# Optimization experiments

Measured on AMD Instinct MI355X. Metric: run time of the kernel, lower is better.

## Reference

```python
import jax, jax.numpy as jnp
import numpy as np

TEMPERATURE = 0.07

def setup_inputs() -> dict:
    key = jax.random.key(0)
    kq, kk = jax.random.split(key)
    B, P, D = 32, 256, 256
    q = jax.random.normal(kq, (B, P, D), dtype=jnp.float32)
    k = jax.random.normal(kk, (B, P, D), dtype=jnp.float32)
    return {"q": q, "k": k}

def reference(q, k):
    B, P, D = q.shape
    inv_t = 1.0 / TEMPERATURE
    k = jax.lax.stop_gradient(k)  # detach_keys=True
    # internal logits: positives on the diagonal of each [P,P] block
    logits = inv_t * jnp.einsum('bid,bjd->bij', q, k)            # [B,P,P]
    # external negatives: cross-batch patch similarities
    ext = inv_t * jnp.einsum('kid,ljd->klij', q, k)              # [B,B,P,P]
    eye = jnp.eye(B, dtype=bool)
    ext = jnp.where(eye[:, :, None, None], -jnp.inf, ext)        # mask same-image blocks
    # rearrange 'b l i j -> b i (l j)'
    ext = ext.transpose(0, 2, 1, 3).reshape(B, P, B * P)
    full = jnp.concatenate([logits, ext], axis=2).reshape(B * P, P + B * P)
    labels = jnp.tile(jnp.arange(P), B)                          # [(B*P)]
    logp = jax.nn.log_softmax(full, axis=-1)
    loss = -jnp.take_along_axis(logp, labels[:, None], axis=1)[:, 0]
    return loss  # [B*P], reduction='none'
```

## Files before the change

kernel.cpp:

```cpp
#include <hip/hip_runtime.h>
#include <hip/hip_bf16.h>

typedef __attribute__((ext_vector_type(8))) short short8;
typedef __attribute__((ext_vector_type(4))) float f32x4;

#define MTOT 8192
#define DDIM 256
#define BM   128
#define BN   32
#define SPLITS 16
#define KPS (MTOT / SPLITS)
#define NIT (KPS / BN)
#define NFRAG (MTOT * 32)

static constexpr float INV_T_F = 14.285714285714286f;
static constexpr float LOG2E   = 1.4426950408889634f;
static constexpr float LN2     = 0.6931471805599453f;
static constexpr float ALPHA   = INV_T_F * LOG2E;

__device__ __forceinline__ unsigned short f2bf(float f) {
    union { float f; unsigned int u; } v; v.f = f;
    unsigned int r = v.u + 0x7fffu + ((v.u >> 16) & 1u);
    return (unsigned short)(r >> 16);
}
#define EXP2R(x) __builtin_amdgcn_exp2f(x)

__global__ void convert_kernel(const float* __restrict__ q, const float* __restrict__ k,
                               short8* __restrict__ qbT, short8* __restrict__ kbT,
                               float* __restrict__ dots) {
    const int g   = blockIdx.x * blockDim.x + threadIdx.x;
    const int row = g >> 5;
    const int c8  = g & 31;
    const float4* q4 = (const float4*)q;
    const float4* k4 = (const float4*)k;
    const float4 qa = q4[(size_t)g * 2], qb = q4[(size_t)g * 2 + 1];
    const float4 ka = k4[(size_t)g * 2], kb = k4[(size_t)g * 2 + 1];

    short8 oq, ok;
    oq[0] = (short)f2bf(qa.x * ALPHA); oq[1] = (short)f2bf(qa.y * ALPHA);
    oq[2] = (short)f2bf(qa.z * ALPHA); oq[3] = (short)f2bf(qa.w * ALPHA);
    oq[4] = (short)f2bf(qb.x * ALPHA); oq[5] = (short)f2bf(qb.y * ALPHA);
    oq[6] = (short)f2bf(qb.z * ALPHA); oq[7] = (short)f2bf(qb.w * ALPHA);
    ok[0] = (short)f2bf(ka.x); ok[1] = (short)f2bf(ka.y);
    ok[2] = (short)f2bf(ka.z); ok[3] = (short)f2bf(ka.w);
    ok[4] = (short)f2bf(kb.x); ok[5] = (short)f2bf(kb.y);
    ok[6] = (short)f2bf(kb.z); ok[7] = (short)f2bf(kb.w);
    const int dst = ((row >> 4) * 8 + (c8 >> 2)) * 64 + (c8 & 3) * 16 + (row & 15);
    qbT[dst] = oq;
    kbT[dst] = ok;

    float d = qa.x * ka.x + qa.y * ka.y + qa.z * ka.z + qa.w * ka.w
            + qb.x * kb.x + qb.y * kb.y + qb.z * kb.z + qb.w * kb.w;
#pragma unroll
    for (int s = 1; s < 32; s <<= 1) d += __shfl_xor(d, s);
    if (c8 == 0) dots[row] = d;
}

__device__ __forceinline__ void stage_chunk(const short8* __restrict__ src_base,
                                            short8* lds_base, int lane) {
#pragma unroll
    for (int i = 0; i < 4; ++i) {
        const short8* g = src_base + i * 64 + lane;
        short8* l = lds_base + i * 64;
        __builtin_amdgcn_global_load_lds(
            (const __attribute__((address_space(1))) unsigned int*)g,
            (__attribute__((address_space(3))) unsigned int*)l,
            16, 0, 0);
    }
}

__global__ __launch_bounds__(256, 3) void flash_lse_kernel(
        const short8* __restrict__ qbT,
        const short8* __restrict__ kbT,
        float* __restrict__ part_m,
        float* __restrict__ part_s) {
    __shared__ short8 smem[2][1024];

    const int mblk  = blockIdx.x;
    const int split = blockIdx.y;
    const int wid   = threadIdx.x >> 6;
    const int lane  = threadIdx.x & 63;
    const int l16   = lane & 15;
    const int lg    = lane >> 4;
    const int rt16  = mblk * 8 + wid * 2;

    short8 qf[2][8];
#pragma unroll
    for (int rt = 0; rt < 2; ++rt)
#pragma unroll
        for (int kk = 0; kk < 8; ++kk)
            qf[rt][kk] = qbT[(size_t)((rt16 + rt) * 8 + kk) * 64 + lane];

    float m_loc[2][4], s_loc[2][4];
#pragma unroll
    for (int rt = 0; rt < 2; ++rt)
#pragma unroll
        for (int j = 0; j < 4; ++j) { m_loc[rt][j] = -1e30f; s_loc[rt][j] = 0.f; }

    const size_t tile_base0 = (size_t)(split * 32) * 512;

    stage_chunk(kbT + tile_base0 + wid * 256, &smem[0][wid * 256], lane);
    __syncthreads();

    for (int it = 0; it < NIT; ++it) {
        const int cur = it & 1;
        if (it + 1 < NIT) {
            const size_t nbase = tile_base0 + (size_t)(it + 1) * 1024;
            stage_chunk(kbT + nbase + wid * 256, &smem[cur ^ 1][wid * 256], lane);
        }

        f32x4 acc[2][2];
#pragma unroll
        for (int rt = 0; rt < 2; ++rt)
#pragma unroll
            for (int ct = 0; ct < 2; ++ct)
                acc[rt][ct] = (f32x4){0.f, 0.f, 0.f, 0.f};

        const short8* sb = smem[cur];
#pragma unroll
        for (int kk = 0; kk < 8; ++kk) {
            short8 bf[2];
#pragma unroll
            for (int ct = 0; ct < 2; ++ct)
                bf[ct] = sb[ct * 512 + kk * 64 + lane];
#pragma unroll
            for (int rt = 0; rt < 2; ++rt)
#pragma unroll
                for (int ct = 0; ct < 2; ++ct)
                    acc[rt][ct] = __builtin_amdgcn_mfma_f32_16x16x32_bf16(
                        qf[rt][kk], bf[ct], acc[rt][ct], 0, 0, 0);
        }

#pragma unroll
        for (int rt = 0; rt < 2; ++rt) {
#pragma unroll
            for (int j = 0; j < 4; ++j) {
                const float x0 = acc[rt][0][j], x1 = acc[rt][1][j];
                const float mo = m_loc[rt][j];
                const float mn = fmaxf(fmaxf(x0, x1), mo);
                float s = s_loc[rt][j] * EXP2R(mo - mn);
                s += EXP2R(x0 - mn) + EXP2R(x1 - mn);
                m_loc[rt][j] = mn;
                s_loc[rt][j] = s;
            }
        }

        __syncthreads();
    }

#pragma unroll
    for (int rt = 0; rt < 2; ++rt) {
#pragma unroll
        for (int j = 0; j < 4; ++j) {
            float m = m_loc[rt][j], s = s_loc[rt][j];
#pragma unroll
            for (int d = 1; d < 16; d <<= 1) {
                const float mo = __shfl_xor(m, d);
                const float so = __shfl_xor(s, d);
                const float mn = fmaxf(m, mo);
                s = s * EXP2R(m - mn) + so * EXP2R(mo - mn);
                m = mn;
            }
            if (l16 == 0) {
                const int row = (rt16 + rt) * 16 + lg * 4 + j;
                part_m[split * MTOT + row] = m;
                part_s[split * MTOT + row] = s;
            }
        }
    }
}

__global__ void combine_kernel(const float* __restrict__ dots,
                               const float* __restrict__ part_m,
                               const float* __restrict__ part_s,
                               float* __restrict__ out) {
    const int tid  = blockIdx.x * blockDim.x + threadIdx.x;
    const int row  = tid >> 4;
    const int l16  = tid & 15;
    float m = part_m[l16 * MTOT + row];
    float s = part_s[l16 * MTOT + row];
#pragma unroll
    for (int d = 1; d < 16; d <<= 1) {
        const float mo = __shfl_xor(m, d);
        const float so = __shfl_xor(s, d);
        const float mn = fmaxf(m, mo);
        s = s * EXP2R(m - mn) + so * EXP2R(mo - mn);
        m = mn;
    }
    if (l16 == 0) {
        out[row] = (m + __log2f(s)) * LN2 - INV_T_F * dots[row];
    }
}

extern "C" void kernel_launch(void* const* d_in, const int* in_sizes, int n_in,
                              void* d_out, int out_size, void* d_ws, size_t ws_size,
                              hipStream_t stream) {
    const float* q = (const float*)d_in[0];
    const float* k = (const float*)d_in[1];
    float* out = (float*)d_out;

    char* ws = (char*)d_ws;
    short8* qbT   = (short8*)ws;
    short8* kbT   = (short8*)(ws + (size_t)NFRAG * 16);
    float* part_m = (float*)(ws + (size_t)NFRAG * 32);
    float* part_s = part_m + SPLITS * MTOT;
    float* dots   = part_s + SPLITS * MTOT;

    convert_kernel<<<NFRAG / 256, 256, 0, stream>>>(q, k, qbT, kbT, dots);
    dim3 grid(MTOT / BM, SPLITS);
    flash_lse_kernel<<<grid, 256, 0, stream>>>(qbT, kbT, part_m, part_s);
    combine_kernel<<<(MTOT * 16) / 256, 256, 0, stream>>>(dots, part_m, part_s, out);
}
```

Before: 106.0 us.

## Double K splits, add lazy max rescaling, and raise MFMA wave priority

Doubles the number of key-dimension splits, so the flash grid has twice as many blocks and each block runs half as many iterations. The combine kernel is widened to merge 32 partials per row. The online softmax now skips the rescale exps unless some row's tile max exceeds its running max by more than 8 (log2 units), accepting bounded growth of the partial sums to save exp work. s_setprio is raised around the MFMA loop to favour the matrix issue. The cost is more partial-result traffic and a larger combine step.

```diff
diff --git a/kernel.cpp b/kernel.cpp
--- a/kernel.cpp
+++ b/kernel.cpp
@@ -8,7 +8,7 @@
 #define DDIM 256
 #define BM   128
 #define BN   32
-#define SPLITS 16
+#define SPLITS 32
 #define KPS (MTOT / SPLITS)
 #define NIT (KPS / BN)
 #define NFRAG (MTOT * 32)
@@ -97,7 +97,7 @@
 #pragma unroll
         for (int j = 0; j < 4; ++j) { m_loc[rt][j] = -1e30f; s_loc[rt][j] = 0.f; }
 
-    const size_t tile_base0 = (size_t)(split * 32) * 512;
+    const size_t tile_base0 = (size_t)split * 8192;
 
     stage_chunk(kbT + tile_base0 + wid * 256, &smem[0][wid * 256], lane);
     __syncthreads();
@@ -117,6 +117,7 @@
                 acc[rt][ct] = (f32x4){0.f, 0.f, 0.f, 0.f};
 
         const short8* sb = smem[cur];
+        __builtin_amdgcn_s_setprio(1);
 #pragma unroll
         for (int kk = 0; kk < 8; ++kk) {
             short8 bf[2];
@@ -130,19 +131,37 @@
                     acc[rt][ct] = __builtin_amdgcn_mfma_f32_16x16x32_bf16(
                         qf[rt][kk], bf[ct], acc[rt][ct], 0, 0, 0);
         }
-
-#pragma unroll
-        for (int rt = 0; rt < 2; ++rt) {
+        __builtin_amdgcn_s_setprio(0);
+
+        float tm[2][4];
+        float gmax = -1e30f;
+#pragma unroll
+        for (int rt = 0; rt < 2; ++rt)
 #pragma unroll
             for (int j = 0; j < 4; ++j) {
-                const float x0 = acc[rt][0][j], x1 = acc[rt][1][j];
-                const float mo = m_loc[rt][j];
-                const float mn = fmaxf(fmaxf(x0, x1), mo);
-                float s = s_loc[rt][j] * EXP2R(mo - mn);
-                s += EXP2R(x0 - mn) + EXP2R(x1 - mn);
-                m_loc[rt][j] = mn;
-                s_loc[rt][j] = s;
+                tm[rt][j] = fmaxf(acc[rt][0][j], acc[rt][1][j]);
+                gmax = fmaxf(gmax, tm[rt][j] - m_loc[rt][j]);
             }
+        if (__any(gmax > 8.0f)) {
+#pragma unroll
+            for (int rt = 0; rt < 2; ++rt)
+#pragma unroll
+                for (int j = 0; j < 4; ++j) {
+                    const float mo = m_loc[rt][j];
+                    const float mn = fmaxf(tm[rt][j], mo);
+                    float s = s_loc[rt][j] * EXP2R(mo - mn);
+                    s += EXP2R(acc[rt][0][j] - mn) + EXP2R(acc[rt][1][j] - mn);
+                    m_loc[rt][j] = mn;
+                    s_loc[rt][j] = s;
+                }
+        } else {
+#pragma unroll
+            for (int rt = 0; rt < 2; ++rt)
+#pragma unroll
+                for (int j = 0; j < 4; ++j) {
+                    const float mo = m_loc[rt][j];
+                    s_loc[rt][j] += EXP2R(acc[rt][0][j] - mo) + EXP2R(acc[rt][1][j] - mo);
+                }
         }
 
         __syncthreads();
@@ -175,19 +194,19 @@
                                const float* __restrict__ part_s,
                                float* __restrict__ out) {
     const int tid  = blockIdx.x * blockDim.x + threadIdx.x;
-    const int row  = tid >> 4;
-    const int l16  = tid & 15;
-    float m = part_m[l16 * MTOT + row];
-    float s = part_s[l16 * MTOT + row];
-#pragma unroll
-    for (int d = 1; d < 16; d <<= 1) {
+    const int row  = tid >> 5;
+    const int l32  = tid & 31;
+    float m = part_m[l32 * MTOT + row];
+    float s = part_s[l32 * MTOT + row];
+#pragma unroll
+    for (int d = 1; d < 32; d <<= 1) {
         const float mo = __shfl_xor(m, d);
         const float so = __shfl_xor(s, d);
         const float mn = fmaxf(m, mo);
         s = s * EXP2R(m - mn) + so * EXP2R(mo - mn);
         m = mn;
     }
-    if (l16 == 0) {
+    if (l32 == 0) {
         out[row] = (m + __log2f(s)) * LN2 - INV_T_F * dots[row];
     }
 }
@@ -209,5 +228,5 @@
     convert_kernel<<<NFRAG / 256, 256, 0, stream>>>(q, k, qbT, kbT, dots);
     dim3 grid(MTOT / BM, SPLITS);
     flash_lse_kernel<<<grid, 256, 0, stream>>>(qbT, kbT, part_m, part_s);
-    combine_kernel<<<(MTOT * 16) / 256, 256, 0, stream>>>(dots, part_m, part_s, out);
-}
+    combine_kernel<<<(MTOT * 32) / 256, 256, 0, stream>>>(dots, part_m, part_s, out);
+}
```

Result: slower. 111.8 us (+5.4%).
